# Performance work log

Measured on AMD Instinct MI355X. Metric: run time of the kernel, lower is better.

## Reference

```python
import jax, jax.numpy as jnp
import numpy as np

B_, S_, E_ = 1, 2048, 2048
NH, P_, N_, G_, K_, CS = 64, 64, 128, 1, 4, 256
INTER = NH * P_            # 4096
CONV_DIM = INTER + 2 * G_ * N_  # 4352
PROJ = INTER + CONV_DIM + NH
EPS = 1e-5


def setup_inputs() -> dict:
    key = jax.random.key(0)
    ks = jax.random.split(key, 6)
    return {
        "input_states": jax.random.normal(ks[0], (B_, S_, E_), dtype=jnp.float32),
        "mask": jnp.ones((B_, 1, S_), dtype=jnp.int32),
        "W_in": jax.random.normal(ks[1], (PROJ, E_), dtype=jnp.float32) * 0.02,
        "conv_w": jax.random.normal(ks[2], (CONV_DIM, K_), dtype=jnp.float32) * 0.2,
        "conv_b": jnp.zeros((CONV_DIM,), dtype=jnp.float32),
        "dt_bias": jnp.ones((NH,), dtype=jnp.float32),
        "A_log": jnp.log(jnp.arange(1, NH + 1, dtype=jnp.float32)),
        "D": jnp.ones((NH,), dtype=jnp.float32),
        "norm_w": jnp.ones((INTER,), dtype=jnp.float32),
        "W_out": jax.random.normal(ks[3], (E_, INTER), dtype=jnp.float32) * 0.02,
    }


def segsum(x):
    # x: [..., L]; out[..., i, j] = sum_{j < k <= i} x[..., k], -inf above diagonal
    L = x.shape[-1]
    i = jnp.arange(L)
    strict = i[:, None] > i[None, :]
    X = jnp.where(strict, x[..., :, None], 0.0)   # [..., L(i), L(j)]
    S = jnp.cumsum(X, axis=-2)
    return jnp.where(i[:, None] >= i[None, :], S, -jnp.inf)


def reference(input_states, mask, W_in, conv_w, conv_b, dt_bias, A_log, D, norm_w, W_out):
    B, S, E = input_states.shape
    # mask has shape[1]==1 -> apply_mask_to_padding_states is a no-op
    proj = input_states @ W_in.T                      # [B,S,PROJ]
    gate = proj[..., :INTER]
    h_BC = proj[..., INTER:INTER + CONV_DIM]
    dt = proj[..., INTER + CONV_DIM:]                 # [B,S,NH]

    # causal depthwise conv1d (padding=K-1, truncated to seq_len)
    xpad = jnp.pad(h_BC, ((0, 0), (K_ - 1, 0), (0, 0)))
    conv = conv_b
    for i in range(K_):
        conv = conv + xpad[:, i:i + S, :] * conv_w[:, i]
    h_BC = jax.nn.silu(conv)

    hidden = h_BC[..., :INTER]
    Bm = h_BC[..., INTER:INTER + G_ * N_]
    Cm = h_BC[..., INTER + G_ * N_:]

    A = -jnp.exp(A_log)                               # [NH]
    dt = jnp.clip(jax.nn.softplus(dt + dt_bias), 0.0) # [B,S,NH]

    Hs = hidden.reshape(B, S, NH, P_).astype(jnp.float32)
    Bm = jnp.tile(Bm.reshape(B, S, G_, N_).astype(jnp.float32), (1, 1, NH // G_, 1))
    Cm = jnp.tile(Cm.reshape(B, S, G_, N_).astype(jnp.float32), (1, 1, NH // G_, 1))

    D_resid = D[None, None, :, None] * Hs             # pad=0 since S % CS == 0
    Hdt = Hs * dt[..., None]
    At = A * dt                                       # [B,S,NH]

    C_ = S // CS
    Hc = Hdt.reshape(B, C_, CS, NH, P_)
    Ac = At.reshape(B, C_, CS, NH)
    Bc = Bm.reshape(B, C_, CS, NH, N_)
    Cc = Cm.reshape(B, C_, CS, NH, N_)

    Ap = jnp.transpose(Ac, (0, 3, 1, 2))              # [B,H,C,L]
    A_cum = jnp.cumsum(Ap, axis=-1)                   # [B,H,C,L]
    L_tri = jnp.exp(segsum(Ap))                       # [B,H,C,L,L]

    # diagonal (intra-chunk) output
    Gm = jnp.einsum('bclhn,bcshn->bclsh', Cc, Bc)
    M = Gm * jnp.transpose(L_tri, (0, 2, 3, 4, 1))    # [B,C,L,S,H]
    Yd = jnp.einsum('bclsh,bcshp->bclhp', M, Hc)

    # per-chunk states (note: source uses same-chunk states, no inter-chunk scan)
    decay = jnp.exp(A_cum[..., -1:] - A_cum)          # [B,H,C,L]
    Bd = Bc * jnp.transpose(decay, (0, 2, 3, 1))[..., None]
    states = jnp.einsum('bclhn,bclhp->bchpn', Bd, Hc) # [B,C,H,P,N]

    Sd = jnp.transpose(jnp.exp(A_cum), (0, 2, 3, 1))  # [B,C,L,H]
    Yoff = jnp.einsum('bclhn,bchpn->bclhp', Cc, states) * Sd[..., None]

    y = (Yd + Yoff).reshape(B, S, NH, P_) + D_resid
    y = y.reshape(B, S, INTER)

    # gated RMSNorm (fp32)
    yf = y.astype(jnp.float32) * jax.nn.silu(gate.astype(jnp.float32))
    var = jnp.mean(yf * yf, axis=-1, keepdims=True)
    yn = norm_w * (yf * jax.lax.rsqrt(var + EPS))

    return yn @ W_out.T
```

## Files before the change

kernel.cpp:

```cpp
#include <hip/hip_runtime.h>
#include <math.h>

#define S_LEN   2048
#define E_DIM   2048
#define NH      64
#define P_DIM   64
#define N_DIM   128
#define CS      256
#define NCHUNK  8
#define INTER   4096
#define CONVD   4352
#define PROJ    8512
#define GEMM1N  8448
#define EPS     1e-5f

#define OFF_PROJBF 0ull
#define OFF_HBC    8650752ull
#define OFF_DTG    17563648ull
#define OFF_DTPART 17694720ull
#define OFF_GM     18743296ull
#define OFF_YV     19267584ull
#define OFF_R      27656192ull

typedef __bf16 bf16x8 __attribute__((ext_vector_type(8)));
typedef float  f32x4  __attribute__((ext_vector_type(4)));
typedef float  f32x16 __attribute__((ext_vector_type(16)));

__device__ __forceinline__ float bf2f(unsigned short u) {
    union { unsigned int i; float f; } v; v.i = ((unsigned int)u) << 16; return v.f;
}
__device__ __forceinline__ unsigned short f2bf(float f) {
    union { float f; unsigned int i; } v; v.f = f;
    unsigned int r = v.i + 0x7FFFu + ((v.i >> 16) & 1u);
    return (unsigned short)(r >> 16);
}
__device__ __forceinline__ void gl_lds16(const void* g, void* l) {
    __builtin_amdgcn_global_load_lds(
        (const __attribute__((address_space(1))) void*)g,
        (__attribute__((address_space(3))) void*)l, 16, 0, 0);
}

__global__ __launch_bounds__(256) void cast_bf16_kernel(
    const float* __restrict__ in, unsigned short* __restrict__ out)
{
    size_t i = ((size_t)blockIdx.x * 256 + threadIdx.x) * 8;
    float4 a = *(const float4*)(in + i);
    float4 b = *(const float4*)(in + i + 4);
    uint4 o;
    o.x = (unsigned int)f2bf(a.x) | ((unsigned int)f2bf(a.y) << 16);
    o.y = (unsigned int)f2bf(a.z) | ((unsigned int)f2bf(a.w) << 16);
    o.z = (unsigned int)f2bf(b.x) | ((unsigned int)f2bf(b.y) << 16);
    o.w = (unsigned int)f2bf(b.z) | ((unsigned int)f2bf(b.w) << 16);
    *(uint4*)(out + i) = o;
}

__global__ __launch_bounds__(256) void gemm_bt_mfma(
    const unsigned short* __restrict__ A, int lda, long long sA,
    const unsigned short* __restrict__ B, int ldb, long long sB,
    float* __restrict__ Cf, unsigned short* __restrict__ Cb, int ldc,
    long long sC, int K)
{
    __shared__ unsigned short As[128 * 64];
    __shared__ unsigned short Bs[128 * 64];
    A += (long long)blockIdx.z * sA;
    B += (long long)blockIdx.z * sB;
    const int t     = threadIdx.x;
    const int m0    = blockIdx.y * 128;
    const int n0    = blockIdx.x * 128;
    const int w     = t >> 6;
    const int lane  = t & 63;
    const int col   = lane & 31;
    const int khalf = lane >> 5;
    const int wm    = (w & 1) * 64;
    const int wn    = (w >> 1) * 64;

    const int srow  = t >> 3;
    const int sslot = t & 7;
    const unsigned short* Agp[4];
    const unsigned short* Bgp[4];
#pragma unroll
    for (int i = 0; i < 4; i++) {
        const int r   = srow + 32 * i;
        const int gch = sslot ^ ((r ^ (r >> 3)) & 7);
        Agp[i] = A + (size_t)(m0 + r) * lda + gch * 8;
        Bgp[i] = B + (size_t)(n0 + r) * ldb + gch * 8;
    }
    unsigned short* Asl = &As[t * 8];
    unsigned short* Bsl = &Bs[t * 8];

    int aOff[2], aXor[2], bOff[2], bXor[2];
#pragma unroll
    for (int i = 0; i < 2; i++) {
        const int ra = wm + i * 32 + col;
        aOff[i] = ra * 64; aXor[i] = (ra ^ (ra >> 3)) & 7;
        const int rb = wn + i * 32 + col;
        bOff[i] = rb * 64; bXor[i] = (rb ^ (rb >> 3)) & 7;
    }

    f32x16 acc[2][2];
#pragma unroll
    for (int mi = 0; mi < 2; mi++)
#pragma unroll
        for (int ni = 0; ni < 2; ni++)
#pragma unroll
            for (int e = 0; e < 16; e++) acc[mi][ni][e] = 0.f;

    for (int k0 = 0; k0 < K; k0 += 64) {
        __syncthreads();
#pragma unroll
        for (int i = 0; i < 4; i++) {
            gl_lds16(Agp[i] + k0, Asl + i * 2048);
            gl_lds16(Bgp[i] + k0, Bsl + i * 2048);
        }
        __syncthreads();
#pragma unroll
        for (int ks = 0; ks < 4; ks++) {
            const int ch = ks * 2 + khalf;
            bf16x8 af[2], bfr[2];
#pragma unroll
            for (int i = 0; i < 2; i++) {
                af[i]  = *(const bf16x8*)&As[aOff[i] + ((ch ^ aXor[i]) * 8)];
                bfr[i] = *(const bf16x8*)&Bs[bOff[i] + ((ch ^ bXor[i]) * 8)];
            }
#pragma unroll
            for (int mi = 0; mi < 2; mi++)
#pragma unroll
                for (int ni = 0; ni < 2; ni++)
                    acc[mi][ni] = __builtin_amdgcn_mfma_f32_32x32x16_bf16(
                        af[mi], bfr[ni], acc[mi][ni], 0, 0, 0);
        }
    }

    if (Cb) {
#pragma unroll
        for (int mi = 0; mi < 2; mi++)
#pragma unroll
            for (int ni = 0; ni < 2; ni++) {
                const int rbase = m0 + wm + mi * 32 + 4 * khalf;
                const int cc    = n0 + wn + ni * 32 + col;
#pragma unroll
                for (int g = 0; g < 4; g++)
#pragma unroll
                    for (int rr = 0; rr < 4; rr++)
                        Cb[(size_t)(rbase + 8 * g + rr) * ldc + cc] =
                            f2bf(acc[mi][ni][4 * g + rr]);
            }
    } else {
        float* Cz = Cf + (long long)blockIdx.z * sC;
#pragma unroll
        for (int mi = 0; mi < 2; mi++)
#pragma unroll
            for (int ni = 0; ni < 2; ni++) {
                const int rbase = m0 + wm + mi * 32 + 4 * khalf;
                const int cc    = n0 + wn + ni * 32 + col;
#pragma unroll
                for (int g = 0; g < 4; g++)
#pragma unroll
                    for (int rr = 0; rr < 4; rr++)
                        Cz[(size_t)(rbase + 8 * g + rr) * ldc + cc] =
                            acc[mi][ni][4 * g + rr];
            }
    }
}

__global__ __launch_bounds__(256) void addf_kernel(
    const float* __restrict__ a, const float* __restrict__ b,
    float* __restrict__ o)
{
    size_t i = ((size_t)blockIdx.x * 256 + threadIdx.x) * 4;
    float4 x = *(const float4*)(a + i);
    float4 y = *(const float4*)(b + i);
    float4 r = make_float4(x.x + y.x, x.y + y.y, x.z + y.z, x.w + y.w);
    *(float4*)(o + i) = r;
}

__global__ __launch_bounds__(256) void gemm_nt(
    const float* __restrict__ A, int lda, long long sA,
    const float* __restrict__ B, int ldb, long long sB,
    float* __restrict__ C, int ldc, long long sC, int K)
{
    A += (long long)blockIdx.z * sA;
    B += (long long)blockIdx.z * sB;
    C += (long long)blockIdx.z * sC;
    const int t  = threadIdx.x;
    const int m0 = blockIdx.y * 128;
    const int n0 = blockIdx.x * 64;
    __shared__ float As[16][132];
    __shared__ float Bs[16][68];
    const int tx = t & 15;
    const int ty = t >> 4;

    const int arow = t & 127;
    const int akh  = (t >> 7) * 8;
    const float* Aload = A + (size_t)(m0 + arow) * (size_t)lda + akh;
    const int brow = t & 63;
    const int bk4  = (t >> 6) * 4;
    const float* Bload = B + (size_t)(n0 + brow) * (size_t)ldb + bk4;

    float acc[8][4];
#pragma unroll
    for (int i = 0; i < 8; i++)
#pragma unroll
        for (int j = 0; j < 4; j++) acc[i][j] = 0.f;

    for (int k0 = 0; k0 < K; k0 += 16) {
        __syncthreads();
        float4 a0 = *(const float4*)(Aload + k0);
        float4 a1 = *(const float4*)(Aload + k0 + 4);
        float4 b0 = *(const float4*)(Bload + k0);
        As[akh + 0][arow] = a0.x; As[akh + 1][arow] = a0.y;
        As[akh + 2][arow] = a0.z; As[akh + 3][arow] = a0.w;
        As[akh + 4][arow] = a1.x; As[akh + 5][arow] = a1.y;
        As[akh + 6][arow] = a1.z; As[akh + 7][arow] = a1.w;
        Bs[bk4 + 0][brow] = b0.x; Bs[bk4 + 1][brow] = b0.y;
        Bs[bk4 + 2][brow] = b0.z; Bs[bk4 + 3][brow] = b0.w;
        __syncthreads();
#pragma unroll
        for (int k = 0; k < 16; k++) {
            float4 a4 = *(const float4*)(&As[k][ty * 8]);
            float4 a5 = *(const float4*)(&As[k][ty * 8 + 4]);
            float4 b4 = *(const float4*)(&Bs[k][tx * 4]);
            float am[8] = {a4.x, a4.y, a4.z, a4.w, a5.x, a5.y, a5.z, a5.w};
            float bn[4] = {b4.x, b4.y, b4.z, b4.w};
#pragma unroll
            for (int i = 0; i < 8; i++)
#pragma unroll
                for (int j = 0; j < 4; j++) acc[i][j] += am[i] * bn[j];
        }
    }
#pragma unroll
    for (int i = 0; i < 8; i++) {
        float4 o = make_float4(acc[i][0], acc[i][1], acc[i][2], acc[i][3]);
        *(float4*)(C + (size_t)(m0 + ty * 8 + i) * (size_t)ldc + n0 + tx * 4) = o;
    }
}

__global__ __launch_bounds__(256) void dt_reduce_kernel(
    const float* __restrict__ part, const float* __restrict__ dt_bias,
    float* __restrict__ dtg)
{
    const int i = blockIdx.x * 256 + threadIdx.x;
    float x = dt_bias[i & 63];
#pragma unroll
    for (int z = 0; z < 8; z++) x += part[(size_t)z * 131072 + i];
    dtg[i] = (x > 20.f) ? x : log1pf(__expf(x));
}

__global__ __launch_bounds__(256) void conv_silu_kernel(
    const unsigned short* __restrict__ projbf, const float* __restrict__ conv_w,
    const float* __restrict__ conv_b, float* __restrict__ out)
{
    const int c = blockIdx.x * 256 + threadIdx.x;
    const int s = blockIdx.y;
    const float4 w = *(const float4*)(conv_w + (size_t)c * 4);
    float acc = conv_b[c];
    const size_t base = 4096 + (size_t)c;
    if (s >= 3) acc += bf2f(projbf[(size_t)(s - 3) * GEMM1N + base]) * w.x;
    if (s >= 2) acc += bf2f(projbf[(size_t)(s - 2) * GEMM1N + base]) * w.y;
    if (s >= 1) acc += bf2f(projbf[(size_t)(s - 1) * GEMM1N + base]) * w.z;
    acc += bf2f(projbf[(size_t)s * GEMM1N + base]) * w.w;
    float sig = 1.f / (1.f + __expf(-acc));
    out[(size_t)s * CONVD + c] = acc * sig;
}

__global__ __launch_bounds__(256, 2) void ssm_mfma_kernel(
    const float* __restrict__ hBC, const float* __restrict__ dtg,
    const float* __restrict__ Gm, const float* __restrict__ A_log,
    const float* __restrict__ Dp, float* __restrict__ y)
{
    const int h    = blockIdx.x;
    const int c    = blockIdx.y;
    const int t    = threadIdx.x;
    const int wid  = t >> 6;
    const int lane = t & 63;
    const int lo   = lane & 15;
    const int q    = lane >> 4;

    __shared__ float sAcum[CS], sdt[CS], sD[CS], sEs[CS], sDecay[CS], sScl[CS];
    __shared__ float sWaveSum[4];
    __shared__ unsigned short sHdtT[64 * 264];
    __shared__ unsigned short sStT[64 * 136];
    __shared__ unsigned short sBufB[128 * 72];

    const float A = -__expf(A_log[h]);
    const int row0 = c * CS;
    const float* hid = hBC + (size_t)row0 * CONVD + h * P_DIM;
    const float* Bp  = hBC + (size_t)row0 * CONVD + INTER;
    const float* Cp  = hBC + (size_t)row0 * CONVD + INTER + N_DIM;
    const float* gm  = Gm + (size_t)c * CS * CS;

    float dtv = dtg[(size_t)(row0 + t) * NH + h];
    float v = A * dtv;
    for (int off = 1; off < 64; off <<= 1) {
        float u = __shfl_up(v, off, 64);
        if (lane >= off) v += u;
    }
    if (lane == 63) sWaveSum[wid] = v;
    __syncthreads();
    float pre = 0.f;
    for (int i = 0; i < 4; i++) if (i < wid) pre += sWaveSum[i];
    v += pre;
    sAcum[t] = v;
    sdt[t] = dtv;
    __syncthreads();
    const float AcumEnd = sAcum[CS - 1];
    {
        float ac   = sAcum[t];
        float apre = (t < 64) ? 0.f : sAcum[(t & ~63) - 1];
        sD[t]     = __expf(ac - apre);
        sEs[t]    = __expf(sAcum[t | 63] - ac);
        sDecay[t] = __expf(AcumEnd - ac);
        sScl[t]   = __expf(ac);
    }

    float* stg = (float*)sStT;
    for (int lt = 0; lt < 4; lt++) {
        __syncthreads();
        {
            const int p4 = (t & 15) * 4;
#pragma unroll
            for (int j = 0; j < 4; j++) {
                int l = (t >> 4) + j * 16;
                *(float4*)&stg[l * 64 + p4] =
                    *(const float4*)(hid + (size_t)(lt * 64 + l) * CONVD + p4);
            }
        }
        __syncthreads();
        {
            const int p = t & 63, lq = (t >> 6) * 16;
#pragma unroll
            for (int j = 0; j < 4; j++) {
                ushort4 pk;
                int l0 = lq + j * 4;
                pk.x = f2bf(stg[(l0 + 0) * 64 + p] * sdt[lt * 64 + l0 + 0]);
                pk.y = f2bf(stg[(l0 + 1) * 64 + p] * sdt[lt * 64 + l0 + 1]);
                pk.z = f2bf(stg[(l0 + 2) * 64 + p] * sdt[lt * 64 + l0 + 2]);
                pk.w = f2bf(stg[(l0 + 3) * 64 + p] * sdt[lt * 64 + l0 + 3]);
                *(uint2*)&sHdtT[p * 264 + lt * 64 + l0] = *(uint2*)&pk;
            }
        }
    }

    f32x4 acc2[2][4];
#pragma unroll
    for (int mi = 0; mi < 2; mi++)
#pragma unroll
        for (int ni = 0; ni < 4; ni++) acc2[mi][ni] = (f32x4){0.f, 0.f, 0.f, 0.f};
    const int psub = (wid & 1) * 32;
    const int nsub = (wid >> 1) * 64;

    for (int qt = 0; qt < 4; qt++) {
        for (int hf = 0; hf < 2; hf++) {
            __syncthreads();
            {
                const int n4 = (t & 31) * 4;
#pragma unroll
                for (int j = 0; j < 4; j++) {
                    int r = (t >> 5) + j * 8;
                    *(float4*)&stg[r * 128 + n4] =
                        *(const float4*)(Bp + (size_t)(qt * 64 + hf * 32 + r) * CONVD + n4);
                }
            }
            __syncthreads();
            {
                const int n = t & 127, lc = (t >> 7) * 16;
#pragma unroll
                for (int j = 0; j < 4; j++) {
                    int l0 = lc + j * 4;
                    ushort4 pk;
                    pk.x = f2bf(stg[(l0 + 0) * 128 + n] * sDecay[qt * 64 + hf * 32 + l0 + 0]);
                    pk.y = f2bf(stg[(l0 + 1) * 128 + n] * sDecay[qt * 64 + hf * 32 + l0 + 1]);
                    pk.z = f2bf(stg[(l0 + 2) * 128 + n] * sDecay[qt * 64 + hf * 32 + l0 + 2]);
                    pk.w = f2bf(stg[(l0 + 3) * 128 + n] * sDecay[qt * 64 + hf * 32 + l0 + 3]);
                    *(uint2*)&sBufB[n * 72 + hf * 32 + l0] = *(uint2*)&pk;
                }
            }
        }
        __syncthreads();
#pragma unroll
        for (int ks = 0; ks < 2; ks++) {
            const int k0 = qt * 64 + ks * 32;
            const int kq = ks * 32;
            bf16x8 a2[2], b2[4];
#pragma unroll
            for (int mi = 0; mi < 2; mi++)
                a2[mi] = *(const bf16x8*)&sHdtT[(psub + mi * 16 + lo) * 264 + k0 + q * 8];
#pragma unroll
            for (int ni = 0; ni < 4; ni++)
                b2[ni] = *(const bf16x8*)&sBufB[(nsub + ni * 16 + lo) * 72 + kq + q * 8];
#pragma unroll
            for (int mi = 0; mi < 2; mi++)
#pragma unroll
                for (int ni = 0; ni < 4; ni++)
                    acc2[mi][ni] = __builtin_amdgcn_mfma_f32_16x16x32_bf16(
                        a2[mi], b2[ni], acc2[mi][ni], 0, 0, 0);
        }
    }
    __syncthreads();
#pragma unroll
    for (int mi = 0; mi < 2; mi++)
#pragma unroll
        for (int ni = 0; ni < 4; ni++)
#pragma unroll
            for (int rr = 0; rr < 4; rr++) {
                int p = psub + mi * 16 + q * 4 + rr;
                int n = nsub + ni * 16 + lo;
                sStT[p * 136 + n] = f2bf(acc2[mi][ni][rr]);
            }

    f32x4 accY[4][2][2];
#pragma unroll
    for (int i = 0; i < 4; i++)
#pragma unroll
        for (int mi = 0; mi < 2; mi++)
#pragma unroll
            for (int pi = 0; pi < 2; pi++) accY[i][mi][pi] = (f32x4){0.f, 0.f, 0.f, 0.f};
    const int pcol = (wid & 1) * 32;
    const int rsub = (wid >> 1) * 16;
    unsigned short* Cs = sBufB;

    for (int i = 0; i < 4; i++) {
        __syncthreads();
        {
            const int n4 = (t & 31) * 4;
#pragma unroll
            for (int j = 0; j < 8; j++) {
                int r = (t >> 5) + j * 8;
                float4 cv = *(const float4*)(Cp + (size_t)(i * 64 + r) * CONVD + n4);
                float scl = sScl[i * 64 + r];
                ushort4 pk;
                pk.x = f2bf(cv.x * scl); pk.y = f2bf(cv.y * scl);
                pk.z = f2bf(cv.z * scl); pk.w = f2bf(cv.w * scl);
                *(uint2*)&Cs[r * 136 + n4] = *(uint2*)&pk;
            }
        }
        __syncthreads();
#pragma unroll
        for (int ks = 0; ks < 4; ks++) {
            const int k0 = ks * 32;
            bf16x8 a3[2], b3[2];
#pragma unroll
            for (int mi = 0; mi < 2; mi++)
                a3[mi] = *(const bf16x8*)&Cs[(mi * 32 + rsub + lo) * 136 + k0 + q * 8];
#pragma unroll
            for (int pi = 0; pi < 2; pi++)
                b3[pi] = *(const bf16x8*)&sStT[(pcol + pi * 16 + lo) * 136 + k0 + q * 8];
#pragma unroll
            for (int mi = 0; mi < 2; mi++)
#pragma unroll
                for (int pi = 0; pi < 2; pi++)
                    accY[i][mi][pi] = __builtin_amdgcn_mfma_f32_16x16x32_bf16(
                        a3[mi], b3[pi], accY[i][mi][pi], 0, 0, 0);
        }
    }

    unsigned short* Mt = sBufB;
    for (int i = 0; i < 4; i++) {
        const int nk = 2 * (i + 1);
        for (int mi = 0; mi < 2; mi++) {
            __syncthreads();
            if (wid <= i) {
                float P = 1.f;
                for (int m = wid + 1; m <= i - 1; m++) P *= sD[m * 64 + 63];
                const int s4 = wid * 64 + lo * 4;
                float4 es4 = *(const float4*)&sEs[s4];
#pragma unroll
                for (int j = 0; j < 8; j++) {
                    int lr = q + j * 4;
                    int l  = i * 64 + mi * 32 + lr;
                    float4 g4 = *(const float4*)&gm[(size_t)l * CS + s4];
                    float w0, w1, w2, w3;
                    if (wid == i) {
                        float al = sAcum[l];
                        w0 = (s4 + 0 <= l) ? __expf(al - sAcum[s4 + 0]) : 0.f;
                        w1 = (s4 + 1 <= l) ? __expf(al - sAcum[s4 + 1]) : 0.f;
                        w2 = (s4 + 2 <= l) ? __expf(al - sAcum[s4 + 2]) : 0.f;
                        w3 = (s4 + 3 <= l) ? __expf(al - sAcum[s4 + 3]) : 0.f;
                    } else {
                        float rs = sD[l] * P;
                        w0 = rs * es4.x; w1 = rs * es4.y;
                        w2 = rs * es4.z; w3 = rs * es4.w;
                    }
                    ushort4 pk;
                    pk.x = f2bf(g4.x * w0); pk.y = f2bf(g4.y * w1);
                    pk.z = f2bf(g4.z * w2); pk.w = f2bf(g4.w * w3);
                    *(uint2*)&Mt[lr * 264 + s4] = *(uint2*)&pk;
                }
            }
            __syncthreads();
            for (int ks = 0; ks < nk; ks++) {
                const int k0 = ks * 32;
                bf16x8 am = *(const bf16x8*)&Mt[(rsub + lo) * 264 + k0 + q * 8];
                bf16x8 b1[2];
#pragma unroll
                for (int pi = 0; pi < 2; pi++)
                    b1[pi] = *(const bf16x8*)&sHdtT[(pcol + pi * 16 + lo) * 264 + k0 + q * 8];
#pragma unroll
                for (int pi = 0; pi < 2; pi++)
                    accY[i][mi][pi] = __builtin_amdgcn_mfma_f32_16x16x32_bf16(
                        am, b1[pi], accY[i][mi][pi], 0, 0, 0);
            }
        }
    }

    const float Dh = Dp[h];
#pragma unroll
    for (int i = 0; i < 4; i++)
#pragma unroll
        for (int mi = 0; mi < 2; mi++)
#pragma unroll
            for (int pi = 0; pi < 2; pi++)
#pragma unroll
                for (int rr = 0; rr < 4; rr++) {
                    int l = i * 64 + mi * 32 + rsub + q * 4 + rr;
                    int p = pcol + pi * 16 + lo;
                    float hv = hid[(size_t)l * CONVD + p];
                    y[(size_t)(row0 + l) * INTER + h * P_DIM + p] =
                        accY[i][mi][pi][rr] + Dh * hv;
                }
}

__global__ __launch_bounds__(256) void norm_kernel(
    const float* __restrict__ y, const unsigned short* __restrict__ projbf,
    const float* __restrict__ norm_w, unsigned short* __restrict__ yn)
{
    const int s = blockIdx.x;
    const int t = threadIdx.x;
    __shared__ float sYf[INTER];
    __shared__ float sW[4];
    const float* yrow = y + (size_t)s * INTER;
    const unsigned short* grow = projbf + (size_t)s * GEMM1N;
    float sum = 0.f;
    for (int j0 = 0; j0 < INTER; j0 += 2048) {
        int j = j0 + t * 8;
        float4 y0 = *(const float4*)(yrow + j);
        float4 y1 = *(const float4*)(yrow + j + 4);
        uint4 gp = *(const uint4*)(grow + j);
        float gv[8] = {
            bf2f((unsigned short)(gp.x & 0xffff)), bf2f((unsigned short)(gp.x >> 16)),
            bf2f((unsigned short)(gp.y & 0xffff)), bf2f((unsigned short)(gp.y >> 16)),
            bf2f((unsigned short)(gp.z & 0xffff)), bf2f((unsigned short)(gp.z >> 16)),
            bf2f((unsigned short)(gp.w & 0xffff)), bf2f((unsigned short)(gp.w >> 16))};
        float yv8[8] = {y0.x, y0.y, y0.z, y0.w, y1.x, y1.y, y1.z, y1.w};
#pragma unroll
        for (int e = 0; e < 8; e++) {
            float f = yv8[e] * (gv[e] / (1.f + __expf(-gv[e])));
            sum += f * f;
            sYf[j + e] = f;
        }
    }
    for (int off = 32; off > 0; off >>= 1) sum += __shfl_down(sum, off, 64);
    if ((t & 63) == 0) sW[t >> 6] = sum;
    __syncthreads();
    const float var = (sW[0] + sW[1] + sW[2] + sW[3]) * (1.f / (float)INTER);
    const float rs = rsqrtf(var + EPS);
    for (int j0 = 0; j0 < INTER; j0 += 2048) {
        int j = j0 + t * 8;
        float4 w0 = *(const float4*)(norm_w + j);
        float4 w1 = *(const float4*)(norm_w + j + 4);
        float wv[8] = {w0.x, w0.y, w0.z, w0.w, w1.x, w1.y, w1.z, w1.w};
        unsigned short o[8];
#pragma unroll
        for (int e = 0; e < 8; e++) o[e] = f2bf(sYf[j + e] * wv[e] * rs);
        uint4 ov;
        ov.x = (unsigned int)o[0] | ((unsigned int)o[1] << 16);
        ov.y = (unsigned int)o[2] | ((unsigned int)o[3] << 16);
        ov.z = (unsigned int)o[4] | ((unsigned int)o[5] << 16);
        ov.w = (unsigned int)o[6] | ((unsigned int)o[7] << 16);
        *(uint4*)(yn + (size_t)s * INTER + j) = ov;
    }
}

extern "C" void kernel_launch(void* const* d_in, const int* in_sizes, int n_in,
                              void* d_out, int out_size, void* d_ws, size_t ws_size,
                              hipStream_t stream)
{
    const float* X       = (const float*)d_in[0];
    const float* W_in    = (const float*)d_in[2];
    const float* conv_w  = (const float*)d_in[3];
    const float* conv_b  = (const float*)d_in[4];
    const float* dt_bias = (const float*)d_in[5];
    const float* A_log   = (const float*)d_in[6];
    const float* Dp      = (const float*)d_in[7];
    const float* norm_w  = (const float*)d_in[8];
    const float* W_out   = (const float*)d_in[9];
    float* out = (float*)d_out;
    float* ws  = (float*)d_ws;

    unsigned short* projbf = (unsigned short*)(ws + OFF_PROJBF);
    float* hbc     = ws + OFF_HBC;
    float* dtg     = ws + OFF_DTG;
    float* dtpart  = ws + OFF_DTPART;
    float* gm      = ws + OFF_GM;
    float* yv      = ws + OFF_YV;
    unsigned short* Xbf    = (unsigned short*)(ws + OFF_R);
    unsigned short* Winbf  = (unsigned short*)(ws + OFF_R + 2097152);
    unsigned short* ynbf   = (unsigned short*)(ws + OFF_R);
    unsigned short* Woutbf = (unsigned short*)(ws + OFF_R + 4194304);
    float* part0 = hbc;
    float* part1 = hbc + 4194304;

    cast_bf16_kernel<<<2048, 256, 0, stream>>>(X, Xbf);
    cast_bf16_kernel<<<8448, 256, 0, stream>>>(W_in, Winbf);

    gemm_bt_mfma<<<dim3(GEMM1N / 128, S_LEN / 128, 1), 256, 0, stream>>>(
        Xbf, E_DIM, 0LL, Winbf, E_DIM, 0LL, nullptr, projbf, GEMM1N, 0LL, E_DIM);

    cast_bf16_kernel<<<4096, 256, 0, stream>>>(W_out, Woutbf);

    gemm_nt<<<dim3(1, 16, 8), 256, 0, stream>>>(
        X, E_DIM, 256LL, W_in + (size_t)GEMM1N * E_DIM, E_DIM, 256LL,
        dtpart, NH, 131072LL, 256);
    dt_reduce_kernel<<<512, 256, 0, stream>>>(dtpart, dt_bias, dtg);

    conv_silu_kernel<<<dim3(CONVD / 256, S_LEN), 256, 0, stream>>>(
        projbf, conv_w, conv_b, hbc);

    gemm_nt<<<dim3(CS / 64, CS / 128, NCHUNK), 256, 0, stream>>>(
        hbc + INTER + N_DIM, CONVD, (long long)CS * CONVD,
        hbc + INTER,         CONVD, (long long)CS * CONVD,
        gm, CS, (long long)CS * CS, N_DIM);

    ssm_mfma_kernel<<<dim3(NH, NCHUNK), 256, 0, stream>>>(
        hbc, dtg, gm, A_log, Dp, yv);

    norm_kernel<<<dim3(S_LEN), 256, 0, stream>>>(yv, projbf, norm_w, ynbf);

    gemm_bt_mfma<<<dim3(E_DIM / 128, S_LEN / 128, 2), 256, 0, stream>>>(
        ynbf, INTER, 2048LL, Woutbf, INTER, 2048LL,
        part0, nullptr, E_DIM, 4194304LL, 2048);
    addf_kernel<<<4096, 256, 0, stream>>>(part0, part1, out);
}
```

Measured before the change: 467.9 us.

## Store conv output in bf16, use MFMA for Gm, split dt GEMM further

The conv+SiLU kernel now produces 8 timesteps per thread, reusing the loaded window, and writes bf16 instead of fp32. The SSM kernel reads bf16 hidden/B/C with wider vector loads. The C·Bᵀ Gm product switches from the fp32 SIMT GEMM to the bf16 MFMA GEMM. The dt projection GEMM gets a finer K split (32 slices), with a matching reduce and reshuffled workspace offsets. This halves intermediate traffic, but bf16 rounding of the conv output adds error to B, C and hidden.

```diff
diff --git a/kernel.cpp b/kernel.cpp
--- a/kernel.cpp
+++ b/kernel.cpp
@@ -16,11 +16,11 @@
 
 #define OFF_PROJBF 0ull
 #define OFF_HBC    8650752ull
-#define OFF_DTG    17563648ull
-#define OFF_DTPART 17694720ull
-#define OFF_GM     18743296ull
-#define OFF_YV     19267584ull
-#define OFF_R      27656192ull
+#define OFF_DTG    13107200ull
+#define OFF_DTPART 13238272ull
+#define OFF_GM     17432576ull
+#define OFF_YV     17956864ull
+#define OFF_R      26345472ull
 
 typedef __bf16 bf16x8 __attribute__((ext_vector_type(8)));
 typedef float  f32x4  __attribute__((ext_vector_type(4)));
@@ -242,29 +242,35 @@
     const int i = blockIdx.x * 256 + threadIdx.x;
     float x = dt_bias[i & 63];
 #pragma unroll
-    for (int z = 0; z < 8; z++) x += part[(size_t)z * 131072 + i];
+    for (int z = 0; z < 32; z++) x += part[(size_t)z * 131072 + i];
     dtg[i] = (x > 20.f) ? x : log1pf(__expf(x));
 }
 
-__global__ __launch_bounds__(256) void conv_silu_kernel(
+__global__ __launch_bounds__(256) void conv_silu8_kernel(
     const unsigned short* __restrict__ projbf, const float* __restrict__ conv_w,
-    const float* __restrict__ conv_b, float* __restrict__ out)
-{
-    const int c = blockIdx.x * 256 + threadIdx.x;
-    const int s = blockIdx.y;
+    const float* __restrict__ conv_b, unsigned short* __restrict__ out)
+{
+    const int c  = blockIdx.x * 256 + threadIdx.x;
+    const int s0 = blockIdx.y * 8;
     const float4 w = *(const float4*)(conv_w + (size_t)c * 4);
-    float acc = conv_b[c];
+    const float b = conv_b[c];
     const size_t base = 4096 + (size_t)c;
-    if (s >= 3) acc += bf2f(projbf[(size_t)(s - 3) * GEMM1N + base]) * w.x;
-    if (s >= 2) acc += bf2f(projbf[(size_t)(s - 2) * GEMM1N + base]) * w.y;
-    if (s >= 1) acc += bf2f(projbf[(size_t)(s - 1) * GEMM1N + base]) * w.z;
-    acc += bf2f(projbf[(size_t)s * GEMM1N + base]) * w.w;
-    float sig = 1.f / (1.f + __expf(-acc));
-    out[(size_t)s * CONVD + c] = acc * sig;
+    float v[11];
+#pragma unroll
+    for (int m = 0; m < 11; m++) {
+        int s = s0 - 3 + m;
+        v[m] = (s >= 0) ? bf2f(projbf[(size_t)s * GEMM1N + base]) : 0.f;
+    }
+#pragma unroll
+    for (int j = 0; j < 8; j++) {
+        float acc = b + v[j] * w.x + v[j + 1] * w.y + v[j + 2] * w.z + v[j + 3] * w.w;
+        float sig = 1.f / (1.f + __expf(-acc));
+        out[(size_t)(s0 + j) * CONVD + c] = f2bf(acc * sig);
+    }
 }
 
 __global__ __launch_bounds__(256, 2) void ssm_mfma_kernel(
-    const float* __restrict__ hBC, const float* __restrict__ dtg,
+    const unsigned short* __restrict__ hBC, const float* __restrict__ dtg,
     const float* __restrict__ Gm, const float* __restrict__ A_log,
     const float* __restrict__ Dp, float* __restrict__ y)
 {
@@ -284,10 +290,10 @@
 
     const float A = -__expf(A_log[h]);
     const int row0 = c * CS;
-    const float* hid = hBC + (size_t)row0 * CONVD + h * P_DIM;
-    const float* Bp  = hBC + (size_t)row0 * CONVD + INTER;
-    const float* Cp  = hBC + (size_t)row0 * CONVD + INTER + N_DIM;
-    const float* gm  = Gm + (size_t)c * CS * CS;
+    const unsigned short* hid = hBC + (size_t)row0 * CONVD + h * P_DIM;
+    const unsigned short* Bp  = hBC + (size_t)row0 * CONVD + INTER;
+    const unsigned short* Cp  = hBC + (size_t)row0 * CONVD + INTER + N_DIM;
+    const float* gm = Gm + (size_t)c * CS * CS;
 
     float dtv = dtg[(size_t)(row0 + t) * NH + h];
     float v = A * dtv;
@@ -313,16 +319,16 @@
         sScl[t]   = __expf(ac);
     }
 
-    float* stg = (float*)sStT;
+    unsigned short* stgu = sStT;
     for (int lt = 0; lt < 4; lt++) {
         __syncthreads();
         {
-            const int p4 = (t & 15) * 4;
-#pragma unroll
-            for (int j = 0; j < 4; j++) {
-                int l = (t >> 4) + j * 16;
-                *(float4*)&stg[l * 64 + p4] =
-                    *(const float4*)(hid + (size_t)(lt * 64 + l) * CONVD + p4);
+            const int c8 = (t & 7) * 8;
+#pragma unroll
+            for (int j = 0; j < 2; j++) {
+                int l = (t >> 3) + 32 * j;
+                *(uint4*)&stgu[l * 64 + c8] =
+                    *(const uint4*)(hid + (size_t)(lt * 64 + l) * CONVD + c8);
             }
         }
         __syncthreads();
@@ -332,10 +338,10 @@
             for (int j = 0; j < 4; j++) {
                 ushort4 pk;
                 int l0 = lq + j * 4;
-                pk.x = f2bf(stg[(l0 + 0) * 64 + p] * sdt[lt * 64 + l0 + 0]);
-                pk.y = f2bf(stg[(l0 + 1) * 64 + p] * sdt[lt * 64 + l0 + 1]);
-                pk.z = f2bf(stg[(l0 + 2) * 64 + p] * sdt[lt * 64 + l0 + 2]);
-                pk.w = f2bf(stg[(l0 + 3) * 64 + p] * sdt[lt * 64 + l0 + 3]);
+                pk.x = f2bf(bf2f(stgu[(l0 + 0) * 64 + p]) * sdt[lt * 64 + l0 + 0]);
+                pk.y = f2bf(bf2f(stgu[(l0 + 1) * 64 + p]) * sdt[lt * 64 + l0 + 1]);
+                pk.z = f2bf(bf2f(stgu[(l0 + 2) * 64 + p]) * sdt[lt * 64 + l0 + 2]);
+                pk.w = f2bf(bf2f(stgu[(l0 + 3) * 64 + p]) * sdt[lt * 64 + l0 + 3]);
                 *(uint2*)&sHdtT[p * 264 + lt * 64 + l0] = *(uint2*)&pk;
             }
         }
@@ -353,12 +359,12 @@
         for (int hf = 0; hf < 2; hf++) {
             __syncthreads();
             {
-                const int n4 = (t & 31) * 4;
-#pragma unroll
-                for (int j = 0; j < 4; j++) {
-                    int r = (t >> 5) + j * 8;
-                    *(float4*)&stg[r * 128 + n4] =
-                        *(const float4*)(Bp + (size_t)(qt * 64 + hf * 32 + r) * CONVD + n4);
+                const int n8 = (t & 15) * 8;
+#pragma unroll
+                for (int j = 0; j < 2; j++) {
+                    int r = (t >> 4) + 16 * j;
+                    *(uint4*)&stgu[r * 128 + n8] =
+                        *(const uint4*)(Bp + (size_t)(qt * 64 + hf * 32 + r) * CONVD + n8);
                 }
             }
             __syncthreads();
@@ -368,10 +374,10 @@
                 for (int j = 0; j < 4; j++) {
                     int l0 = lc + j * 4;
                     ushort4 pk;
-                    pk.x = f2bf(stg[(l0 + 0) * 128 + n] * sDecay[qt * 64 + hf * 32 + l0 + 0]);
-                    pk.y = f2bf(stg[(l0 + 1) * 128 + n] * sDecay[qt * 64 + hf * 32 + l0 + 1]);
-                    pk.z = f2bf(stg[(l0 + 2) * 128 + n] * sDecay[qt * 64 + hf * 32 + l0 + 2]);
-                    pk.w = f2bf(stg[(l0 + 3) * 128 + n] * sDecay[qt * 64 + hf * 32 + l0 + 3]);
+                    pk.x = f2bf(bf2f(stgu[(l0 + 0) * 128 + n]) * sDecay[qt * 64 + hf * 32 + l0 + 0]);
+                    pk.y = f2bf(bf2f(stgu[(l0 + 1) * 128 + n]) * sDecay[qt * 64 + hf * 32 + l0 + 1]);
+                    pk.z = f2bf(bf2f(stgu[(l0 + 2) * 128 + n]) * sDecay[qt * 64 + hf * 32 + l0 + 2]);
+                    pk.w = f2bf(bf2f(stgu[(l0 + 3) * 128 + n]) * sDecay[qt * 64 + hf * 32 + l0 + 3]);
                     *(uint2*)&sBufB[n * 72 + hf * 32 + l0] = *(uint2*)&pk;
                 }
             }
@@ -422,16 +428,20 @@
     for (int i = 0; i < 4; i++) {
         __syncthreads();
         {
-            const int n4 = (t & 31) * 4;
-#pragma unroll
-            for (int j = 0; j < 8; j++) {
-                int r = (t >> 5) + j * 8;
-                float4 cv = *(const float4*)(Cp + (size_t)(i * 64 + r) * CONVD + n4);
+            const int n8 = (t & 15) * 8;
+#pragma unroll
+            for (int j = 0; j < 4; j++) {
+                int r = (t >> 4) + 16 * j;
+                uint4 cv = *(const uint4*)(Cp + (size_t)(i * 64 + r) * CONVD + n8);
                 float scl = sScl[i * 64 + r];
-                ushort4 pk;
-                pk.x = f2bf(cv.x * scl); pk.y = f2bf(cv.y * scl);
-                pk.z = f2bf(cv.z * scl); pk.w = f2bf(cv.w * scl);
-                *(uint2*)&Cs[r * 136 + n4] = *(uint2*)&pk;
+                const unsigned short* cu = (const unsigned short*)&cv;
+                ushort4 p0, p1;
+                p0.x = f2bf(bf2f(cu[0]) * scl); p0.y = f2bf(bf2f(cu[1]) * scl);
+                p0.z = f2bf(bf2f(cu[2]) * scl); p0.w = f2bf(bf2f(cu[3]) * scl);
+                p1.x = f2bf(bf2f(cu[4]) * scl); p1.y = f2bf(bf2f(cu[5]) * scl);
+                p1.z = f2bf(bf2f(cu[6]) * scl); p1.w = f2bf(bf2f(cu[7]) * scl);
+                *(uint2*)&Cs[r * 136 + n8]     = *(uint2*)&p0;
+                *(uint2*)&Cs[r * 136 + n8 + 4] = *(uint2*)&p1;
             }
         }
         __syncthreads();
@@ -514,7 +524,7 @@
                 for (int rr = 0; rr < 4; rr++) {
                     int l = i * 64 + mi * 32 + rsub + q * 4 + rr;
                     int p = pcol + pi * 16 + lo;
-                    float hv = hid[(size_t)l * CONVD + p];
+                    float hv = bf2f(hid[(size_t)l * CONVD + p]);
                     y[(size_t)(row0 + l) * INTER + h * P_DIM + p] =
                         accY[i][mi][pi][rr] + Dh * hv;
                 }
@@ -588,7 +598,7 @@
     float* ws  = (float*)d_ws;
 
     unsigned short* projbf = (unsigned short*)(ws + OFF_PROJBF);
-    float* hbc     = ws + OFF_HBC;
+    unsigned short* hbc16  = (unsigned short*)(ws + OFF_HBC);
     float* dtg     = ws + OFF_DTG;
     float* dtpart  = ws + OFF_DTPART;
     float* gm      = ws + OFF_GM;
@@ -597,8 +607,8 @@
     unsigned short* Winbf  = (unsigned short*)(ws + OFF_R + 2097152);
     unsigned short* ynbf   = (unsigned short*)(ws + OFF_R);
     unsigned short* Woutbf = (unsigned short*)(ws + OFF_R + 4194304);
-    float* part0 = hbc;
-    float* part1 = hbc + 4194304;
+    float* part0 = ws + OFF_PROJBF;
+    float* part1 = part0 + 4194304;
 
     cast_bf16_kernel<<<2048, 256, 0, stream>>>(X, Xbf);
     cast_bf16_kernel<<<8448, 256, 0, stream>>>(W_in, Winbf);
@@ -608,21 +618,21 @@
 
     cast_bf16_kernel<<<4096, 256, 0, stream>>>(W_out, Woutbf);
 
-    gemm_nt<<<dim3(1, 16, 8), 256, 0, stream>>>(
-        X, E_DIM, 256LL, W_in + (size_t)GEMM1N * E_DIM, E_DIM, 256LL,
-        dtpart, NH, 131072LL, 256);
+    gemm_nt<<<dim3(1, 16, 32), 256, 0, stream>>>(
+        X, E_DIM, 64LL, W_in + (size_t)GEMM1N * E_DIM, E_DIM, 64LL,
+        dtpart, NH, 131072LL, 64);
     dt_reduce_kernel<<<512, 256, 0, stream>>>(dtpart, dt_bias, dtg);
 
-    conv_silu_kernel<<<dim3(CONVD / 256, S_LEN), 256, 0, stream>>>(
-        projbf, conv_w, conv_b, hbc);
-
-    gemm_nt<<<dim3(CS / 64, CS / 128, NCHUNK), 256, 0, stream>>>(
-        hbc + INTER + N_DIM, CONVD, (long long)CS * CONVD,
-        hbc + INTER,         CONVD, (long long)CS * CONVD,
-        gm, CS, (long long)CS * CS, N_DIM);
+    conv_silu8_kernel<<<dim3(CONVD / 256, S_LEN / 8), 256, 0, stream>>>(
+        projbf, conv_w, conv_b, hbc16);
+
+    gemm_bt_mfma<<<dim3(CS / 128, CS / 128, NCHUNK), 256, 0, stream>>>(
+        hbc16 + INTER + N_DIM, CONVD, (long long)CS * CONVD,
+        hbc16 + INTER,         CONVD, (long long)CS * CONVD,
+        gm, nullptr, CS, (long long)CS * CS, N_DIM);
 
     ssm_mfma_kernel<<<dim3(NH, NCHUNK), 256, 0, stream>>>(
-        hbc, dtg, gm, A_log, Dp, yv);
+        hbc16, dtg, gm, A_log, Dp, yv);
 
     norm_kernel<<<dim3(S_LEN), 256, 0, stream>>>(yv, projbf, norm_w, ynbf);
 
```

Result: faster. 424.4 us (-9.3%).
